# Kernel optimization log

Hardware: AMD Instinct MI355X
Metric: run time of the kernel (lower is better)

## Reference

```python
import jax, jax.numpy as jnp
import numpy as np

H = 1024      # hidden_size
NH = 16       # num_heads
HD = H // NH  # head_dim


def setup_inputs() -> dict:
    key = jax.random.key(0)
    ks = jax.random.split(key, 5)
    x = jax.random.normal(ks[0], (2, 2048, H), dtype=jnp.float32)
    # nn.Linear weights are [out, in]; keep that convention
    w_qkv = jax.random.normal(ks[1], (3 * H, H), dtype=jnp.float32) * (1.0 / np.sqrt(H))
    b_qkv = jax.random.normal(ks[2], (3 * H,), dtype=jnp.float32) * 0.01
    w_out = jax.random.normal(ks[3], (H, H), dtype=jnp.float32) * (1.0 / np.sqrt(H))
    b_out = jax.random.normal(ks[4], (H,), dtype=jnp.float32) * 0.01
    return {"x": x, "w_qkv": w_qkv, "b_qkv": b_qkv, "w_out": w_out, "b_out": b_out}


def reference(x, w_qkv, b_qkv, w_out, b_out):
    B, L, _ = x.shape
    scale = HD ** -0.5
    qkv = x @ w_qkv.T + b_qkv                       # [B,L,3H]
    qkv = qkv.reshape(B, L, 3, NH, HD).transpose(2, 0, 3, 1, 4)  # [3,B,NH,L,HD]
    q, k, v = qkv[0], qkv[1], qkv[2]
    attn = jnp.einsum('bhqd,bhkd->bhqk', q, k) * scale
    attn = jax.nn.softmax(attn, axis=-1)            # dropout is identity in eval
    out = jnp.einsum('bhqk,bhkd->bhqd', attn, v)    # [B,NH,L,HD]
    out = out.transpose(0, 2, 1, 3).reshape(B, L, H)
    return out @ w_out.T + b_out
```

## Files before the change

### kernel.cpp

```cpp
#include <hip/hip_runtime.h>
#include <hip/hip_bf16.h>
#include <stdint.h>

#define H_DIM  1024
#define NHEADS 16
#define HDIM   64
#define BATCH  2
#define SEQ    2048
#define MROWS  (BATCH * SEQ)
#define QKV_N  (3 * H_DIM)
#define QK_LD  (2 * H_DIM)
#define NT     (SEQ / 64)

typedef __attribute__((ext_vector_type(8))) __bf16 bf16x8;
typedef __attribute__((ext_vector_type(4))) float  floatx4;

__device__ __forceinline__ unsigned short f2bf(float f) {
    uint32_t u = __float_as_uint(f);
    u += 0x7fffu + ((u >> 16) & 1u);
    return (unsigned short)(u >> 16);
}
__device__ __forceinline__ float bf2f(unsigned short u) {
    return __uint_as_float(((uint32_t)u) << 16);
}
__device__ __forceinline__ uint32_t cvtpk_bf16(float lo, float hi) {
    uint32_t r;
    asm("v_cvt_pk_bf16_f32 %0, %1, %2" : "=v"(r) : "v"(lo), "v"(hi));
    return r;
}

#if __has_builtin(__builtin_amdgcn_exp2f)
#define fexp2 __builtin_amdgcn_exp2f
#else
#define fexp2 exp2f
#endif

__device__ __forceinline__ void async_ld16(const void* g, void* l) {
    __builtin_amdgcn_global_load_lds(
        (const __attribute__((address_space(1))) void*)g,
        (__attribute__((address_space(3))) void*)l, 16, 0, 0);
}

__global__ __launch_bounds__(256) void cvt_f32_bf16(const float4* __restrict__ in,
                                                    ushort4* __restrict__ out, int n4) {
    int i = blockIdx.x * 256 + threadIdx.x;
    if (i < n4) {
        float4 v = in[i];
        ushort4 o;
        o.x = f2bf(v.x); o.y = f2bf(v.y); o.z = f2bf(v.z); o.w = f2bf(v.w);
        out[i] = o;
    }
}

__global__ __launch_bounds__(256) void gemm_bt(const unsigned short* __restrict__ A,
                                               const unsigned short* __restrict__ B,
                                               const float* __restrict__ bias,
                                               unsigned short* __restrict__ Cb,
                                               float* __restrict__ Cf,
                                               unsigned short* __restrict__ Vt,
                                               int ldc, int Kdim) {
    __shared__ __align__(16) unsigned short As[128 * 64];
    __shared__ __align__(16) unsigned short Bs[128 * 64];
    const int tid  = threadIdx.x;
    const int lane = tid & 63;
    const int wave = tid >> 6;
    const int waveM = (wave >> 1) * 64;
    const int waveN = (wave & 1) * 64;
    const int bm = blockIdx.y, bn = blockIdx.x;

    floatx4 acc[4][4];
    #pragma unroll
    for (int i = 0; i < 4; ++i)
        #pragma unroll
        for (int j = 0; j < 4; ++j) {
            floatx4 z = {0.f, 0.f, 0.f, 0.f};
            acc[i][j] = z;
        }

    int rr[4], kc[4];
    #pragma unroll
    for (int i = 0; i < 4; ++i) {
        int c = i * 256 + tid;
        rr[i] = c >> 3;
        kc[i] = ((c & 7) ^ (rr[i] & 7)) * 8;
    }

    const int lr = lane & 15;
    const int g  = lane >> 4;
    const int sw = lr & 7;

    for (int k0 = 0; k0 < Kdim; k0 += 64) {
        #pragma unroll
        for (int i = 0; i < 4; ++i) {
            async_ld16(&A[(size_t)(bm * 128 + rr[i]) * Kdim + k0 + kc[i]],
                       (char*)As + i * 4096 + wave * 1024);
            async_ld16(&B[(size_t)(bn * 128 + rr[i]) * Kdim + k0 + kc[i]],
                       (char*)Bs + i * 4096 + wave * 1024);
        }
        __syncthreads();

        #pragma unroll
        for (int kk = 0; kk < 2; ++kk) {
            const int gk = (((kk << 2) + g) ^ sw) * 8;
            bf16x8 af[4], bfr[4];
            #pragma unroll
            for (int i = 0; i < 4; ++i)
                af[i] = *(const bf16x8*)&As[(waveM + i * 16 + lr) * 64 + gk];
            #pragma unroll
            for (int j = 0; j < 4; ++j)
                bfr[j] = *(const bf16x8*)&Bs[(waveN + j * 16 + lr) * 64 + gk];

            #pragma unroll
            for (int i = 0; i < 4; ++i)
                #pragma unroll
                for (int j = 0; j < 4; ++j)
                    acc[i][j] = __builtin_amdgcn_mfma_f32_16x16x32_bf16(af[i], bfr[j], acc[i][j], 0, 0, 0);
        }
        __syncthreads();
    }

    const int crow0 = bm * 128 + waveM + (lane >> 4) * 4;
    const int ccol0 = bn * 128 + waveN + (lane & 15);
    #pragma unroll
    for (int i = 0; i < 4; ++i)
        #pragma unroll
        for (int j = 0; j < 4; ++j) {
            int col = ccol0 + j * 16;
            float bv = bias[col];
            #pragma unroll
            for (int r = 0; r < 4; ++r) {
                int row = crow0 + i * 16 + r;
                float v = acc[i][j][r] + bv;
                if (Vt && col >= 2 * H_DIM) {
                    int hd = col - 2 * H_DIM;
                    int bb = row >> 11, kv = row & (SEQ - 1);
                    int hh = hd >> 6,  dd = hd & 63;
                    Vt[((size_t)((bb << 4) + hh) * HDIM + dd) * SEQ + kv] = f2bf(v);
                } else if (Cb) {
                    Cb[(size_t)row * ldc + col] = f2bf(v);
                } else {
                    Cf[(size_t)row * ldc + col] = v;
                }
            }
        }
}

__global__ __launch_bounds__(256) void gemm_bt64(const unsigned short* __restrict__ A,
                                                 const unsigned short* __restrict__ B,
                                                 const float* __restrict__ bias,
                                                 float* __restrict__ Cf,
                                                 int ldc, int Kdim) {
    __shared__ __align__(16) unsigned short As[128 * 64];
    __shared__ __align__(16) unsigned short Bs[64 * 64];
    const int tid  = threadIdx.x;
    const int lane = tid & 63;
    const int wave = tid >> 6;
    const int waveM = wave * 32;
    const int bm = blockIdx.y, bn = blockIdx.x;

    floatx4 acc[2][4];
    #pragma unroll
    for (int i = 0; i < 2; ++i)
        #pragma unroll
        for (int j = 0; j < 4; ++j) {
            floatx4 z = {0.f, 0.f, 0.f, 0.f};
            acc[i][j] = z;
        }

    int rr[4], kc[4];
    #pragma unroll
    for (int i = 0; i < 4; ++i) {
        int c = i * 256 + tid;
        rr[i] = c >> 3;
        kc[i] = ((c & 7) ^ (rr[i] & 7)) * 8;
    }

    const int lr = lane & 15;
    const int g  = lane >> 4;
    const int sw = lr & 7;

    for (int k0 = 0; k0 < Kdim; k0 += 64) {
        #pragma unroll
        for (int i = 0; i < 4; ++i)
            async_ld16(&A[(size_t)(bm * 128 + rr[i]) * Kdim + k0 + kc[i]],
                       (char*)As + i * 4096 + wave * 1024);
        #pragma unroll
        for (int i = 0; i < 2; ++i)
            async_ld16(&B[(size_t)(bn * 64 + rr[i]) * Kdim + k0 + kc[i]],
                       (char*)Bs + i * 4096 + wave * 1024);
        __syncthreads();

        #pragma unroll
        for (int kk = 0; kk < 2; ++kk) {
            const int gk = (((kk << 2) + g) ^ sw) * 8;
            bf16x8 af[2], bfr[4];
            #pragma unroll
            for (int i = 0; i < 2; ++i)
                af[i] = *(const bf16x8*)&As[(waveM + i * 16 + lr) * 64 + gk];
            #pragma unroll
            for (int j = 0; j < 4; ++j)
                bfr[j] = *(const bf16x8*)&Bs[(j * 16 + lr) * 64 + gk];

            #pragma unroll
            for (int i = 0; i < 2; ++i)
                #pragma unroll
                for (int j = 0; j < 4; ++j)
                    acc[i][j] = __builtin_amdgcn_mfma_f32_16x16x32_bf16(af[i], bfr[j], acc[i][j], 0, 0, 0);
        }
        __syncthreads();
    }

    const int crow0 = bm * 128 + waveM + (lane >> 4) * 4;
    const int ccol0 = bn * 64 + (lane & 15);
    #pragma unroll
    for (int i = 0; i < 2; ++i)
        #pragma unroll
        for (int j = 0; j < 4; ++j) {
            int col = ccol0 + j * 16;
            float bv = bias[col];
            #pragma unroll
            for (int r = 0; r < 4; ++r) {
                int row = crow0 + i * 16 + r;
                Cf[(size_t)row * ldc + col] = acc[i][j][r] + bv;
            }
        }
}

__global__ __launch_bounds__(256, 4) void attn_mfma(const unsigned short* __restrict__ qkv2,
                                                    const unsigned short* __restrict__ vt,
                                                    unsigned short* __restrict__ ctx) {
    __shared__ __align__(16) unsigned short Ks2[2][64 * 64];
    __shared__ __align__(16) unsigned short Vt2[2][64 * 64];

    const int tid  = threadIdx.x;
    const int lane = tid & 63;
    const int wave = tid >> 6;
    const int bh = blockIdx.y;
    const int b  = bh >> 4, h = bh & 15;
    const int q0 = blockIdx.x * 64 + wave * 16;
    const int lq = lane & 15;
    const int g  = lane >> 4;
    const int swz = lq & 7;

    const float QS = 0.125f * 1.44269504f;
    bf16x8 qf[2];
    #pragma unroll
    for (int kk = 0; kk < 2; ++kk) {
        union { bf16x8 v; unsigned short u[8]; } tq;
        tq.v = *(const bf16x8*)&qkv2[(size_t)(b * SEQ + q0 + lq) * QK_LD
                                     + h * HDIM + kk * 32 + g * 8];
        #pragma unroll
        for (int e = 0; e < 8; ++e) tq.u[e] = f2bf(bf2f(tq.u[e]) * QS);
        qf[kk] = tq.v;
    }

    floatx4 acc_o[4];
    #pragma unroll
    for (int j = 0; j < 4; ++j) {
        floatx4 z = {0.f, 0.f, 0.f, 0.f};
        acc_o[j] = z;
    }
    float l_run = 0.f;

    const unsigned short* gK = qkv2 + (size_t)b * SEQ * QK_LD + H_DIM + (size_t)h * HDIM;
    const unsigned short* gV = vt + (size_t)bh * HDIM * SEQ;

    const int r0  = tid >> 3;
    const int pr0 = (r0 & 32) | ((r0 & 12) << 1) | ((r0 & 16) >> 2) | (r0 & 3);
    const int gs0 = (tid & 7) ^ (r0 & 7);
    const unsigned short* pK0 = gK + (size_t)pr0 * QK_LD + gs0 * 8;
    const unsigned short* pK1 = gK + (size_t)(pr0 + 32) * QK_LD + gs0 * 8;
    const unsigned short* pV0 = gV + (size_t)r0 * SEQ + gs0 * 8;
    const unsigned short* pV1 = gV + (size_t)(r0 + 32) * SEQ + gs0 * 8;

    #define STAGE_KV(bi)                                                        \
        {                                                                       \
            async_ld16(pK0, (char*)&Ks2[bi][0] + (wave * 64) * 16);             \
            async_ld16(pK1, (char*)&Ks2[bi][0] + (256 + wave * 64) * 16);       \
            async_ld16(pV0, (char*)&Vt2[bi][0] + (wave * 64) * 16);             \
            async_ld16(pV1, (char*)&Vt2[bi][0] + (256 + wave * 64) * 16);       \
            pK0 += 64 * QK_LD; pK1 += 64 * QK_LD; pV0 += 64; pV1 += 64;         \
        }

    STAGE_KV(0)
    __syncthreads();

    int buf = 0;
    for (int t = 0; t < NT; ++t) {
        if (t + 1 < NT) STAGE_KV(buf ^ 1)

        const unsigned short* Ksb = &Ks2[buf][0];
        const unsigned short* Vsb = &Vt2[buf][0];

        bf16x8 kf[4][2];
        #pragma unroll
        for (int jb = 0; jb < 4; ++jb)
            #pragma unroll
            for (int kk = 0; kk < 2; ++kk)
                kf[jb][kk] = *(const bf16x8*)&Ksb[(jb * 16 + lq) * 64 + (((kk << 2) + g) ^ swz) * 8];

        bf16x8 vf[4][2];
        #pragma unroll
        for (int dt = 0; dt < 4; ++dt)
            #pragma unroll
            for (int kk = 0; kk < 2; ++kk)
                vf[dt][kk] = *(const bf16x8*)&Vsb[(dt * 16 + lq) * 64 + (((kk << 2) + g) ^ swz) * 8];

        __builtin_amdgcn_sched_barrier(0);

        floatx4 sa[4];
        #pragma unroll
        for (int jb = 0; jb < 4; ++jb) {
            floatx4 z = {0.f, 0.f, 0.f, 0.f};
            sa[jb] = z;
        }
        __builtin_amdgcn_s_setprio(1);
        #pragma unroll
        for (int jb = 0; jb < 4; ++jb)
            #pragma unroll
            for (int kk = 0; kk < 2; ++kk)
                sa[jb] = __builtin_amdgcn_mfma_f32_16x16x32_bf16(kf[jb][kk], qf[kk], sa[jb], 0, 0, 0);
        __builtin_amdgcn_s_setprio(0);

        float ps = 0.f;

        {
            float e00 = fexp2(sa[0][0]), e01 = fexp2(sa[0][1]), e02 = fexp2(sa[0][2]), e03 = fexp2(sa[0][3]);
            float e10 = fexp2(sa[1][0]), e11 = fexp2(sa[1][1]), e12 = fexp2(sa[1][2]), e13 = fexp2(sa[1][3]);
            ps += ((e00 + e01) + (e02 + e03)) + ((e10 + e11) + (e12 + e13));
            union { bf16x8 v; uint32_t u[4]; } pf;
            pf.u[0] = cvtpk_bf16(e00, e01); pf.u[1] = cvtpk_bf16(e02, e03);
            pf.u[2] = cvtpk_bf16(e10, e11); pf.u[3] = cvtpk_bf16(e12, e13);
            __builtin_amdgcn_s_setprio(1);
            #pragma unroll
            for (int dt = 0; dt < 4; ++dt)
                acc_o[dt] = __builtin_amdgcn_mfma_f32_16x16x32_bf16(pf.v, vf[dt][0], acc_o[dt], 0, 0, 0);
            __builtin_amdgcn_s_setprio(0);
        }

        {
            float e00 = fexp2(sa[2][0]), e01 = fexp2(sa[2][1]), e02 = fexp2(sa[2][2]), e03 = fexp2(sa[2][3]);
            float e10 = fexp2(sa[3][0]), e11 = fexp2(sa[3][1]), e12 = fexp2(sa[3][2]), e13 = fexp2(sa[3][3]);
            ps += ((e00 + e01) + (e02 + e03)) + ((e10 + e11) + (e12 + e13));
            union { bf16x8 v; uint32_t u[4]; } pf;
            pf.u[0] = cvtpk_bf16(e00, e01); pf.u[1] = cvtpk_bf16(e02, e03);
            pf.u[2] = cvtpk_bf16(e10, e11); pf.u[3] = cvtpk_bf16(e12, e13);
            __builtin_amdgcn_s_setprio(1);
            #pragma unroll
            for (int dt = 0; dt < 4; ++dt)
                acc_o[dt] = __builtin_amdgcn_mfma_f32_16x16x32_bf16(pf.v, vf[dt][1], acc_o[dt], 0, 0, 0);
            __builtin_amdgcn_s_setprio(0);
        }

        ps += __shfl_xor(ps, 16);
        ps += __shfl_xor(ps, 32);
        l_run += ps;

        __syncthreads();
        buf ^= 1;
    }
    #undef STAGE_KV

    float linv[4];
    #pragma unroll
    for (int r = 0; r < 4; ++r)
        linv[r] = 1.f / __shfl(l_run, g * 4 + r);
    #pragma unroll
    for (int dt = 0; dt < 4; ++dt)
        #pragma unroll
        for (int r = 0; r < 4; ++r)
            ctx[(size_t)(b * SEQ + q0 + g * 4 + r) * H_DIM + h * HDIM + dt * 16 + lq]
                = f2bf(acc_o[dt][r] * linv[r]);
}

extern "C" void kernel_launch(void* const* d_in, const int* in_sizes, int n_in,
                              void* d_out, int out_size, void* d_ws, size_t ws_size,
                              hipStream_t stream) {
    const float* x     = (const float*)d_in[0];
    const float* w_qkv = (const float*)d_in[1];
    const float* b_qkv = (const float*)d_in[2];
    const float* w_out = (const float*)d_in[3];
    const float* b_out = (const float*)d_in[4];
    float* out = (float*)d_out;

    unsigned short* xb    = (unsigned short*)d_ws;
    unsigned short* wqkvb = xb    + (size_t)MROWS * H_DIM;
    unsigned short* woutb = wqkvb + (size_t)QKV_N * H_DIM;
    unsigned short* qkv2  = woutb + (size_t)H_DIM * H_DIM;
    unsigned short* ctxb  = qkv2  + (size_t)MROWS * QK_LD;
    unsigned short* vtb   = ctxb  + (size_t)MROWS * H_DIM;

    cvt_f32_bf16<<<MROWS * H_DIM / 1024, 256, 0, stream>>>((const float4*)x,     (ushort4*)xb,    MROWS * H_DIM / 4);
    cvt_f32_bf16<<<QKV_N * H_DIM / 1024, 256, 0, stream>>>((const float4*)w_qkv, (ushort4*)wqkvb, QKV_N * H_DIM / 4);
    cvt_f32_bf16<<<H_DIM * H_DIM / 1024, 256, 0, stream>>>((const float4*)w_out, (ushort4*)woutb, H_DIM * H_DIM / 4);

    gemm_bt<<<dim3(QKV_N / 128, MROWS / 128), 256, 0, stream>>>(xb, wqkvb, b_qkv, qkv2, nullptr, vtb, QK_LD, H_DIM);

    attn_mfma<<<dim3(SEQ / 64, BATCH * NHEADS), 256, 0, stream>>>(qkv2, vtb, ctxb);

    gemm_bt64<<<dim3(H_DIM / 64, MROWS / 128), 256, 0, stream>>>(ctxb, woutb, b_out, out, H_DIM, H_DIM);
}
```

Baseline: 194.7 us.

## Fuse conversions, write V row-major then transpose, swizzle GEMM workgroup order

Merges the three fp32-to-bf16 conversion launches into one kernel. The QKV GEMM epilogue now writes V in coalesced row-major order into a scratch buffer, and a separate LDS-tiled kernel transposes it into the head-major Vt layout, replacing the scattered strided stores. Both GEMMs remap workgroup IDs so that consecutive blocks are spread across XCD-sized groups, aiming for better L2 locality. The cost is one extra kernel launch and an extra read and write pass over V. The ctx buffer is reused as V scratch, which is safe because attention overwrites it only after the transpose has run.

```diff
diff --git a/kernel.cpp b/kernel.cpp
--- a/kernel.cpp
+++ b/kernel.cpp
@@ -41,15 +41,51 @@
         (__attribute__((address_space(3))) void*)l, 16, 0, 0);
 }
 
-__global__ __launch_bounds__(256) void cvt_f32_bf16(const float4* __restrict__ in,
-                                                    ushort4* __restrict__ out, int n4) {
+#define N4_X   (MROWS * H_DIM / 4)
+#define N4_WQ  (QKV_N * H_DIM / 4)
+#define N4_WO  (H_DIM * H_DIM / 4)
+__global__ __launch_bounds__(256) void cvt_all(const float4* __restrict__ x,
+                                               const float4* __restrict__ wq,
+                                               const float4* __restrict__ wo,
+                                               ushort4* __restrict__ xb,
+                                               ushort4* __restrict__ wqb,
+                                               ushort4* __restrict__ wob) {
     int i = blockIdx.x * 256 + threadIdx.x;
-    if (i < n4) {
-        float4 v = in[i];
-        ushort4 o;
-        o.x = f2bf(v.x); o.y = f2bf(v.y); o.z = f2bf(v.z); o.w = f2bf(v.w);
-        out[i] = o;
-    }
+    const float4* in;
+    ushort4* out;
+    int j;
+    if (i < N4_X)                { in = x;  out = xb;  j = i; }
+    else if (i < N4_X + N4_WQ)   { in = wq; out = wqb; j = i - N4_X; }
+    else                         { in = wo; out = wob; j = i - N4_X - N4_WQ; }
+    float4 v = in[j];
+    ushort4 o;
+    o.x = f2bf(v.x); o.y = f2bf(v.y); o.z = f2bf(v.z); o.w = f2bf(v.w);
+    out[j] = o;
+}
+
+__global__ __launch_bounds__(256) void transpose_v(const unsigned short* __restrict__ vr,
+                                                   unsigned short* __restrict__ vt) {
+    __shared__ unsigned short T[64][72];
+    const int tid = threadIdx.x;
+    const int bh = blockIdx.y;
+    const int b = bh >> 4, h = bh & 15;
+    const int kv0 = blockIdx.x * 64;
+    const int r  = tid >> 2, cs = (tid & 3) * 16;
+
+    const unsigned short* src = &vr[(size_t)(b * SEQ + kv0 + r) * H_DIM + h * HDIM + cs];
+    union { uint4 q; unsigned short u[8]; } A0, A1;
+    A0.q = *(const uint4*)&src[0];
+    A1.q = *(const uint4*)&src[8];
+    #pragma unroll
+    for (int e = 0; e < 8; ++e) T[cs + e][r]     = A0.u[e];
+    #pragma unroll
+    for (int e = 0; e < 8; ++e) T[cs + 8 + e][r] = A1.u[e];
+    __syncthreads();
+
+    const int dd = tid >> 2, ks = (tid & 3) * 16;
+    unsigned short* dst = &vt[((size_t)bh * HDIM + dd) * SEQ + kv0 + ks];
+    *(uint4*)&dst[0] = *(const uint4*)&T[dd][ks];
+    *(uint4*)&dst[8] = *(const uint4*)&T[dd][ks + 8];
 }
 
 __global__ __launch_bounds__(256) void gemm_bt(const unsigned short* __restrict__ A,
@@ -57,7 +93,7 @@
                                                const float* __restrict__ bias,
                                                unsigned short* __restrict__ Cb,
                                                float* __restrict__ Cf,
-                                               unsigned short* __restrict__ Vt,
+                                               unsigned short* __restrict__ Vr,
                                                int ldc, int Kdim) {
     __shared__ __align__(16) unsigned short As[128 * 64];
     __shared__ __align__(16) unsigned short Bs[128 * 64];
@@ -66,7 +102,11 @@
     const int wave = tid >> 6;
     const int waveM = (wave >> 1) * 64;
     const int waveN = (wave & 1) * 64;
-    const int bm = blockIdx.y, bn = blockIdx.x;
+
+    const int nwg = gridDim.x * gridDim.y;
+    int wg = blockIdx.y * gridDim.x + blockIdx.x;
+    wg = (wg & 7) * (nwg >> 3) + (wg >> 3);
+    const int bm = wg / gridDim.x, bn = wg % gridDim.x;
 
     floatx4 acc[4][4];
     #pragma unroll
@@ -131,11 +171,8 @@
             for (int r = 0; r < 4; ++r) {
                 int row = crow0 + i * 16 + r;
                 float v = acc[i][j][r] + bv;
-                if (Vt && col >= 2 * H_DIM) {
-                    int hd = col - 2 * H_DIM;
-                    int bb = row >> 11, kv = row & (SEQ - 1);
-                    int hh = hd >> 6,  dd = hd & 63;
-                    Vt[((size_t)((bb << 4) + hh) * HDIM + dd) * SEQ + kv] = f2bf(v);
+                if (Vr && col >= 2 * H_DIM) {
+                    Vr[(size_t)row * H_DIM + (col - 2 * H_DIM)] = f2bf(v);
                 } else if (Cb) {
                     Cb[(size_t)row * ldc + col] = f2bf(v);
                 } else {
@@ -156,7 +193,11 @@
     const int lane = tid & 63;
     const int wave = tid >> 6;
     const int waveM = wave * 32;
-    const int bm = blockIdx.y, bn = blockIdx.x;
+
+    const int nwg = gridDim.x * gridDim.y;
+    int wg = blockIdx.y * gridDim.x + blockIdx.x;
+    wg = (wg & 7) * (nwg >> 3) + (wg >> 3);
+    const int bm = wg / gridDim.x, bn = wg % gridDim.x;
 
     floatx4 acc[2][4];
     #pragma unroll
@@ -389,12 +430,15 @@
     unsigned short* qkv2  = woutb + (size_t)H_DIM * H_DIM;
     unsigned short* ctxb  = qkv2  + (size_t)MROWS * QK_LD;
     unsigned short* vtb   = ctxb  + (size_t)MROWS * H_DIM;
-
-    cvt_f32_bf16<<<MROWS * H_DIM / 1024, 256, 0, stream>>>((const float4*)x,     (ushort4*)xb,    MROWS * H_DIM / 4);
-    cvt_f32_bf16<<<QKV_N * H_DIM / 1024, 256, 0, stream>>>((const float4*)w_qkv, (ushort4*)wqkvb, QKV_N * H_DIM / 4);
-    cvt_f32_bf16<<<H_DIM * H_DIM / 1024, 256, 0, stream>>>((const float4*)w_out, (ushort4*)woutb, H_DIM * H_DIM / 4);
-
-    gemm_bt<<<dim3(QKV_N / 128, MROWS / 128), 256, 0, stream>>>(xb, wqkvb, b_qkv, qkv2, nullptr, vtb, QK_LD, H_DIM);
+    unsigned short* vrows = ctxb;
+
+    cvt_all<<<(N4_X + N4_WQ + N4_WO) / 256, 256, 0, stream>>>(
+        (const float4*)x, (const float4*)w_qkv, (const float4*)w_out,
+        (ushort4*)xb, (ushort4*)wqkvb, (ushort4*)woutb);
+
+    gemm_bt<<<dim3(QKV_N / 128, MROWS / 128), 256, 0, stream>>>(xb, wqkvb, b_qkv, qkv2, nullptr, vrows, QK_LD, H_DIM);
+
+    transpose_v<<<dim3(SEQ / 64, BATCH * NHEADS), 256, 0, stream>>>(vrows, vtb);
 
     attn_mfma<<<dim3(SEQ / 64, BATCH * NHEADS), 256, 0, stream>>>(qkv2, vtb, ctxb);
 
```

Measured after the change: 189.7 us. -2.6%, faster.
